# Optimization experiments

Hardware: AMD Instinct MI355X
Metric: run time of the kernel (lower is better)

Reference implementation:

```python
import jax, jax.numpy as jnp
import numpy as np

PAD_TOKEN = 0

def setup_inputs() -> dict:
    key = jax.random.key(0)
    ks = jax.random.split(key, 6)
    B, S, E, W, V = 16, 2048, 128, 128, 7
    x = jax.random.randint(ks[0], (B, S), 0, V, dtype=jnp.int64)
    emb_table = jax.random.normal(ks[1], (V, E), dtype=jnp.float32)
    fc_w = jax.random.normal(ks[2], (E, W * E), dtype=jnp.float32) * 0.02
    fc_b = jax.random.normal(ks[3], (E,), dtype=jnp.float32) * 0.02
    out_w = jax.random.normal(ks[4], (1, E), dtype=jnp.float32) * 0.02
    out_b = jax.random.normal(ks[5], (1,), dtype=jnp.float32) * 0.02
    return {"x": x, "emb_table": emb_table, "fc_w": fc_w, "fc_b": fc_b,
            "out_w": out_w, "out_b": out_b}

def reference(x, emb_table, fc_w, fc_b, out_w, out_b):
    B, S = x.shape
    V, E = emb_table.shape
    Eo, WE = fc_w.shape
    W = WE // E
    # embedding lookup: [B, S, E]
    ex = emb_table[x]
    # causal left pad by W-1 along seq -> [B, S+W-1, E]
    padded = jnp.pad(ex, ((0, 0), (W - 1, 0), (0, 0)))
    # torch unfold gives windows[b,s,e,k] = padded[b, s+k, e], flattened index e*W + k.
    # Equivalent implicit conv: kernel[k, e, o] = fc_w[o, e*W + k]  (WIO layout)
    kernel = jnp.transpose(fc_w.reshape(Eo, E, W), (2, 1, 0))
    conv = jax.lax.conv_general_dilated(
        padded, kernel, window_strides=(1,), padding='VALID',
        dimension_numbers=('NWC', 'WIO', 'NWC'))  # [B, S, Eo]
    h = conv + fc_b
    # output_layer: Linear(E -> 1), then squeeze -> [B, S]
    logits = jnp.einsum('bse,oe->bso', h, out_w)[..., 0] + out_b[0]
    # return_last_seq=True: gather at last non-pad count index
    last_idx = jnp.sum(x != PAD_TOKEN, axis=-1) - 1  # [B]
    out = logits[jnp.arange(B), last_idx].reshape(-1, 1)
    return out
```

## Files before the change

### kernel.cpp

```cpp
#include <hip/hip_runtime.h>

#define BB 16
#define SS 2048
#define EE 128
#define WW 128
#define VV 7
#define WE (WW * EE)

__global__ __launch_bounds__(256) void k1_reduce_w(const float* __restrict__ fc_w,
                                                   const float* __restrict__ out_w,
                                                   float* __restrict__ v_part) {
    __shared__ float red[8][128];
    const int bid = blockIdx.x;
    const int oh = bid >> 7;
    const int ib = bid & 127;
    const int t = threadIdx.x;
    const int og = t >> 5;
    const int il = t & 31;
    const int i = ib * 128 + il * 4;
    const int o0 = oh * 64 + og * 8;

    float4 acc = make_float4(0.f, 0.f, 0.f, 0.f);
#pragma unroll
    for (int oo = 0; oo < 8; ++oo) {
        const int o = o0 + oo;
        const float w = out_w[o];
        const float4 f = *reinterpret_cast<const float4*>(fc_w + (size_t)o * WE + i);
        acc.x += w * f.x;
        acc.y += w * f.y;
        acc.z += w * f.z;
        acc.w += w * f.w;
    }
    *reinterpret_cast<float4*>(&red[og][il * 4]) = acc;
    __syncthreads();
    if (t < 128) {
        float s = 0.f;
#pragma unroll
        for (int g = 0; g < 8; ++g) s += red[g][t];
        v_part[oh * WE + ib * 128 + t] = s;
    }
}

__global__ __launch_bounds__(256) void k2_final(const int* __restrict__ x,
                                                const float* __restrict__ emb,
                                                const float* __restrict__ fc_b,
                                                const float* __restrict__ out_w,
                                                const float* __restrict__ out_b,
                                                const float* __restrict__ v_part,
                                                float* __restrict__ out) {
    __shared__ float embT[EE * 8];
    __shared__ float wred[4];
    __shared__ int cred[4];
    __shared__ int s_last;

    const int b = blockIdx.x;
    const int t = threadIdx.x;
    const int lane = t & 63;
    const int wid = t >> 6;
    const int* xb = x + b * SS;

    for (int idx = t; idx < EE * 8; idx += 256) {
        const int tok = idx & 7;
        const int e = idx >> 3;
        embT[idx] = (tok < VV) ? emb[tok * EE + e] : 0.f;
    }

    int cnt = 0;
#pragma unroll
    for (int r = 0; r < SS / 256; ++r) cnt += (xb[r * 256 + t] != 0) ? 1 : 0;
#pragma unroll
    for (int off = 32; off; off >>= 1) cnt += __shfl_down(cnt, off, 64);
    if (lane == 0) cred[wid] = cnt;
    __syncthreads();
    if (t == 0) s_last = cred[0] + cred[1] + cred[2] + cred[3] - 1;
    __syncthreads();
    const int last = s_last;

    const int k = t & 127;
    const int eh = t >> 7;
    const int j = last - (WW - 1) + k;
    const int tok = (j >= 0) ? xb[j] : VV;
    float acc = 0.f;
    const float* vp = v_part + k;
    const float* er = embT + tok;
#pragma unroll 8
    for (int e = eh * 64; e < eh * 64 + 64; ++e) {
        const float v = vp[e * 128] + vp[WE + e * 128];
        acc += er[e * 8] * v;
    }
    if (t < 128) acc += out_w[t] * fc_b[t];

#pragma unroll
    for (int off = 32; off; off >>= 1) acc += __shfl_down(acc, off, 64);
    if (lane == 0) wred[wid] = acc;
    __syncthreads();
    if (t == 0) out[b] = wred[0] + wred[1] + wred[2] + wred[3] + out_b[0];
}

extern "C" void kernel_launch(void* const* d_in, const int* in_sizes, int n_in,
                              void* d_out, int out_size, void* d_ws, size_t ws_size,
                              hipStream_t stream) {
    const int* x = (const int*)d_in[0];
    const float* emb = (const float*)d_in[1];
    const float* fc_w = (const float*)d_in[2];
    const float* fc_b = (const float*)d_in[3];
    const float* out_w = (const float*)d_in[4];
    const float* out_b = (const float*)d_in[5];
    float* v_part = (float*)d_ws;
    float* out = (float*)d_out;

    k1_reduce_w<<<256, 256, 0, stream>>>(fc_w, out_w, v_part);
    k2_final<<<BB, 256, 0, stream>>>(x, emb, fc_b, out_w, out_b, v_part, out);
}
```

Before: 76.25 us.

## Fuse weight reduction and final gather into one kernel with flag-based sync

Replaces the two-kernel pipeline with a single 256-block kernel. The first 16 blocks compute per-batch last indices, write window tokens and seed the output with the bias term, then publish a sentinel flag. Every block reduces its slice of fc_w against out_w and spins until all flags are set. It then combines its slice with the tokens and embeddings and atomically adds its contribution to the output. This removes the second launch and the serial 16-block gather, at the cost of a cross-block spin wait and atomics. The flags are never reset, so on repeated calls later blocks may skip the wait and atomically add before out is reinitialised, which is a race.

```diff
diff --git a/kernel.cpp b/kernel.cpp
--- a/kernel.cpp
+++ b/kernel.cpp
@@ -6,95 +6,110 @@
 #define WW 128
 #define VV 7
 #define WE (WW * EE)
+#define SENT 0x5A5A5A5A
 
-__global__ __launch_bounds__(256) void k1_reduce_w(const float* __restrict__ fc_w,
-                                                   const float* __restrict__ out_w,
-                                                   float* __restrict__ v_part) {
-    __shared__ float red[8][128];
-    const int bid = blockIdx.x;
-    const int oh = bid >> 7;
-    const int ib = bid & 127;
-    const int t = threadIdx.x;
-    const int og = t >> 5;
-    const int il = t & 31;
-    const int i = ib * 128 + il * 4;
-    const int o0 = oh * 64 + og * 8;
-
-    float4 acc = make_float4(0.f, 0.f, 0.f, 0.f);
-#pragma unroll
-    for (int oo = 0; oo < 8; ++oo) {
-        const int o = o0 + oo;
-        const float w = out_w[o];
-        const float4 f = *reinterpret_cast<const float4*>(fc_w + (size_t)o * WE + i);
-        acc.x += w * f.x;
-        acc.y += w * f.y;
-        acc.z += w * f.z;
-        acc.w += w * f.w;
-    }
-    *reinterpret_cast<float4*>(&red[og][il * 4]) = acc;
-    __syncthreads();
-    if (t < 128) {
-        float s = 0.f;
-#pragma unroll
-        for (int g = 0; g < 8; ++g) s += red[g][t];
-        v_part[oh * WE + ib * 128 + t] = s;
-    }
-}
-
-__global__ __launch_bounds__(256) void k2_final(const int* __restrict__ x,
-                                                const float* __restrict__ emb,
-                                                const float* __restrict__ fc_b,
-                                                const float* __restrict__ out_w,
-                                                const float* __restrict__ out_b,
-                                                const float* __restrict__ v_part,
-                                                float* __restrict__ out) {
-    __shared__ float embT[EE * 8];
-    __shared__ float wred[4];
+__global__ __launch_bounds__(256) void fused(const int* __restrict__ x,
+                                             const float* __restrict__ emb,
+                                             const float* __restrict__ fc_w,
+                                             const float* __restrict__ fc_b,
+                                             const float* __restrict__ out_w,
+                                             const float* __restrict__ out_b,
+                                             int* __restrict__ flags,
+                                             int* __restrict__ w_tok,
+                                             float* __restrict__ out) {
+    __shared__ float red[16][64];
+    __shared__ float v[64];
+    __shared__ float embS[8];
+    __shared__ float tmp2[4];
     __shared__ int cred[4];
     __shared__ int s_last;
 
-    const int b = blockIdx.x;
+    const int bid = blockIdx.x;
     const int t = threadIdx.x;
     const int lane = t & 63;
-    const int wid = t >> 6;
-    const int* xb = x + b * SS;
+    const int w = t >> 6;
 
-    for (int idx = t; idx < EE * 8; idx += 256) {
-        const int tok = idx & 7;
-        const int e = idx >> 3;
-        embT[idx] = (tok < VV) ? emb[tok * EE + e] : 0.f;
+    if (bid < BB) {
+        const int b = bid;
+        const int* xb = x + b * SS;
+        int cnt = 0;
+#pragma unroll
+        for (int r = 0; r < SS / 256; ++r) cnt += (xb[r * 256 + t] != 0) ? 1 : 0;
+#pragma unroll
+        for (int off = 32; off; off >>= 1) cnt += __shfl_down(cnt, off, 64);
+        if (lane == 0) cred[w] = cnt;
+        float p = (t < EE) ? out_w[t] * fc_b[t] : 0.f;
+#pragma unroll
+        for (int off = 32; off; off >>= 1) p += __shfl_down(p, off, 64);
+        if (lane == 0) tmp2[w] = p;
+        __syncthreads();
+        if (t == 0) s_last = cred[0] + cred[1] + cred[2] + cred[3] - 1;
+        __syncthreads();
+        const int last = s_last;
+        if (t < WW) {
+            const int j = last - (WW - 1) + t;
+            w_tok[b * WW + t] = (j >= 0) ? xb[j] : VV;
+        }
+        if (t == 0) out[b] = tmp2[0] + tmp2[1] + tmp2[2] + tmp2[3] + out_b[0];
+        __syncthreads();
+        if (t == 0) {
+            __threadfence();
+            atomicExch(&flags[b], SENT);
+        }
     }
 
-    int cnt = 0;
+    const int e = bid >> 1;
+    const int k0 = (bid & 1) * 64;
+    if (t >= 64 && t < 72) {
+        const int tok = t - 64;
+        embS[tok] = (tok < VV) ? emb[tok * EE + e] : 0.f;
+    }
+    const int oo = lane >> 4;
+    const int kq = lane & 15;
+    const float* fbase = fc_w + (size_t)e * WW + k0 + kq * 4;
+    float4 acc = make_float4(0.f, 0.f, 0.f, 0.f);
 #pragma unroll
-    for (int r = 0; r < SS / 256; ++r) cnt += (xb[r * 256 + t] != 0) ? 1 : 0;
+    for (int it = 0; it < 8; ++it) {
+        const int o = w * 32 + it * 4 + oo;
+        const float ow = out_w[o];
+        const float4 f = *reinterpret_cast<const float4*>(fbase + (size_t)o * WE);
+        acc.x += ow * f.x;
+        acc.y += ow * f.y;
+        acc.z += ow * f.z;
+        acc.w += ow * f.w;
+    }
+    *reinterpret_cast<float4*>(&red[w * 4 + oo][kq * 4]) = acc;
+    __syncthreads();
+    if (t < 64) {
+        float s = 0.f;
 #pragma unroll
-    for (int off = 32; off; off >>= 1) cnt += __shfl_down(cnt, off, 64);
-    if (lane == 0) cred[wid] = cnt;
+        for (int g = 0; g < 16; ++g) s += red[g][t];
+        v[t] = s;
+    }
+
+    if (t == 0) {
+        volatile int* vf = flags;
+        for (;;) {
+            int ok = 1;
+            for (int b2 = 0; b2 < BB; ++b2)
+                if (vf[b2] != SENT) { ok = 0; break; }
+            if (ok) break;
+            __builtin_amdgcn_s_sleep(2);
+        }
+    }
     __syncthreads();
-    if (t == 0) s_last = cred[0] + cred[1] + cred[2] + cred[3] - 1;
-    __syncthreads();
-    const int last = s_last;
+    __threadfence();
 
-    const int k = t & 127;
-    const int eh = t >> 7;
-    const int j = last - (WW - 1) + k;
-    const int tok = (j >= 0) ? xb[j] : VV;
-    float acc = 0.f;
-    const float* vp = v_part + k;
-    const float* er = embT + tok;
-#pragma unroll 8
-    for (int e = eh * 64; e < eh * 64 + 64; ++e) {
-        const float v = vp[e * 128] + vp[WE + e * 128];
-        acc += er[e * 8] * v;
-    }
-    if (t < 128) acc += out_w[t] * fc_b[t];
-
+    const int b = t >> 4;
+    const int kg = t & 15;
+    const int4 tk = *reinterpret_cast<const int4*>(w_tok + b * WW + k0 + kg * 4);
+    float val = v[kg * 4 + 0] * embS[tk.x]
+              + v[kg * 4 + 1] * embS[tk.y]
+              + v[kg * 4 + 2] * embS[tk.z]
+              + v[kg * 4 + 3] * embS[tk.w];
 #pragma unroll
-    for (int off = 32; off; off >>= 1) acc += __shfl_down(acc, off, 64);
-    if (lane == 0) wred[wid] = acc;
-    __syncthreads();
-    if (t == 0) out[b] = wred[0] + wred[1] + wred[2] + wred[3] + out_b[0];
+    for (int off = 8; off; off >>= 1) val += __shfl_down(val, off, 16);
+    if (kg == 0) atomicAdd(&out[b], val);
 }
 
 extern "C" void kernel_launch(void* const* d_in, const int* in_sizes, int n_in,
@@ -106,9 +121,9 @@
     const float* fc_b = (const float*)d_in[3];
     const float* out_w = (const float*)d_in[4];
     const float* out_b = (const float*)d_in[5];
-    float* v_part = (float*)d_ws;
+    int* flags = (int*)d_ws;
+    int* w_tok = flags + BB;
     float* out = (float*)d_out;
 
-    k1_reduce_w<<<256, 256, 0, stream>>>(fc_w, out_w, v_part);
-    k2_final<<<BB, 256, 0, stream>>>(x, emb, fc_b, out_w, out_b, v_part, out);
+    fused<<<256, 256, 0, stream>>>(x, emb, fc_w, fc_b, out_w, out_b, flags, w_tok, out);
 }
```

Result: slower. 100.1 us (+31.3%).
